# Kernel tuning notes

Hardware: AMD Instinct MI355X
Metric: run time of the kernel (lower is better)

## Reference

```python
import jax, jax.numpy as jnp
import numpy as np

KS = 3          # kernel_size
M = 6           # num_bases
TEM = 6         # tem_size = (KS//2)*num_bases
BN_EPS = 1e-3   # keras BatchNormalization default epsilon


def _conv(x, w):
    # x: NCHW, w: OIHW, stride 1, SAME padding (module uses padding='same')
    return jax.lax.conv_general_dilated(x, w, (1, 1), 'SAME',
                                        dimension_numbers=('NCHW', 'OIHW', 'NCHW'))


def _bn(x, gamma, beta, mean, var):
    # inference-mode batchnorm over channel dim (NCHW)
    s = gamma * jax.lax.rsqrt(var + BN_EPS)
    return x * s[None, :, None, None] + (beta - mean * s)[None, :, None, None]


def _unfold(x):
    # im2col: N,C,H,W -> N,C,KS*KS,H,W with SAME padding, stride 1
    N, C, H, W = x.shape
    xp = jnp.pad(x, ((0, 0), (0, 0), (1, 1), (1, 1)))
    taps = [xp[:, :, i:i + H, j:j + W] for i in range(KS) for j in range(KS)]
    return jnp.stack(taps, axis=2)


def setup_inputs() -> dict:
    key = jax.random.key(0)
    ks = jax.random.split(key, 16)
    N, C, O, H, W = 16, 128, 128, 64, 64
    inter, bsz = 64, M * TEM  # 64, 36
    x = jax.random.normal(ks[0], (N, C, H, W), jnp.float32)
    w1 = jax.random.normal(ks[1], (inter, C, 3, 3), jnp.float32) * (1.0 / np.sqrt(C * 9))
    gamma1 = jnp.ones((inter,), jnp.float32)
    beta1 = jnp.zeros((inter,), jnp.float32)
    mean1 = jax.random.normal(ks[2], (inter,), jnp.float32) * 0.1
    var1 = jax.random.uniform(ks[3], (inter,), jnp.float32, 0.5, 1.5)
    w2 = jax.random.normal(ks[4], (bsz, inter, 3, 3), jnp.float32) * (1.0 / np.sqrt(inter * 9))
    gamma2 = jnp.ones((bsz,), jnp.float32)
    beta2 = jnp.zeros((bsz,), jnp.float32)
    mean2 = jax.random.normal(ks[5], (bsz,), jnp.float32) * 0.1
    var2 = jax.random.uniform(ks[6], (bsz,), jnp.float32, 0.5, 1.5)
    # Fixed Fourier-Bessel-style basis [TEM, KS*KS], normalized as in calculate_FB_bases
    rng = np.random.RandomState(0)
    psi = rng.normal(size=(KS * KS, TEM)).astype(np.float32)
    c = np.sqrt((psi ** 2).sum(0).mean())
    fb_bases = jnp.asarray((psi / c).T)  # [TEM, 9]
    coef = jax.random.normal(ks[7], (O, C * M), jnp.float32) * np.sqrt(2.0 / (C * M))
    bias = jnp.zeros((O,), jnp.float32)
    return {'x': x, 'w1': w1, 'gamma1': gamma1, 'beta1': beta1, 'mean1': mean1,
            'var1': var1, 'w2': w2, 'gamma2': gamma2, 'beta2': beta2,
            'mean2': mean2, 'var2': var2, 'fb_bases': fb_bases, 'coef': coef,
            'bias': bias}


def reference(x, w1, gamma1, beta1, mean1, var1, w2, gamma2, beta2, mean2, var2,
              fb_bases, coef, bias):
    N, C, H, W = x.shape
    # bases_net: conv3x3 -> BN -> tanh -> conv3x3 -> BN -> tanh
    h = jnp.tanh(_bn(_conv(x, w1), gamma1, beta1, mean1, var1))
    b = jnp.tanh(_bn(_conv(h, w2), gamma2, beta2, mean2, var2))   # N,36,H,W
    bcoef = b.reshape(N, M, TEM, H, W)
    # combine predicted coefficients with fixed FB bases -> per-pixel filters
    bases = jnp.einsum('bmkhw,kl->bmlhw', bcoef, fb_bases)        # N,M,9,H,W
    xu = _unfold(x)                                               # N,C,9,H,W
    # per-pixel gather-multiply-reduce over the 9 taps
    bo = jnp.einsum('bmlhw,bclhw->bcmhw', bases, xu)              # N,C,M,H,W
    bo = bo.reshape(N, C * M, H, W)
    # 1x1 conv with coef + bias
    out = jnp.einsum('bkhw,ok->bohw', bo, coef) + bias[None, :, None, None]
    return out
```

## Files before the change

### kernel.cpp

```cpp
#include <hip/hip_runtime.h>
#include <hip/hip_bf16.h>

using bf16 = __hip_bfloat16;
typedef __attribute__((ext_vector_type(8))) short bf16x8;
typedef __attribute__((ext_vector_type(4))) float f32x4;
typedef __attribute__((ext_vector_type(2))) float f32x2;

#define BN_EPS 1e-3f

#define OFF_W1M   16u
#define OFF_B1F   36880u
#define OFF_W2M   36944u
#define OFF_B2F   50768u
#define OFF_FBF   50804u
#define OFF_CFM   50860u
#define OFF_BIASF 100012u
#define OFF_BB    100144u

__device__ __forceinline__ int dtype_flag(const void* g1) {
    return ((const unsigned*)g1)[0] != 0x3F800000u;
}

__device__ __forceinline__ float b2f(bf16 v) { return __bfloat162float(v); }
__device__ __forceinline__ unsigned short f2b(float f) {
    union { bf16 h; unsigned short u; } cv;
    cv.h = __float2bfloat16(f);
    return cv.u;
}
__device__ __forceinline__ unsigned packbf(float a, float b) {
    return (unsigned)f2b(a) | ((unsigned)f2b(b) << 16);
}
__device__ __forceinline__ float ldin(const void* p, long long i, int f) {
    return f ? b2f(((const bf16*)p)[i]) : ((const float*)p)[i];
}
__device__ __forceinline__ float lo_f(unsigned u) { return __uint_as_float(u << 16); }
__device__ __forceinline__ float hi_f(unsigned u) { return __uint_as_float(u & 0xFFFF0000u); }
__device__ __forceinline__ void ld8f(const void* p, long long i, int f, float* o) {
    if (f) {
        uint4 v = *(const uint4*)((const unsigned short*)p + i);
        o[0] = lo_f(v.x); o[1] = hi_f(v.x); o[2] = lo_f(v.y); o[3] = hi_f(v.y);
        o[4] = lo_f(v.z); o[5] = hi_f(v.z); o[6] = lo_f(v.w); o[7] = hi_f(v.w);
    } else {
        const float* q = (const float*)p + i;
        float4 a = *(const float4*)q, b = *(const float4*)(q + 4);
        o[0] = a.x; o[1] = a.y; o[2] = a.z; o[3] = a.w;
        o[4] = b.x; o[5] = b.y; o[6] = b.z; o[7] = b.w;
    }
}
__device__ __forceinline__ bf16x8 lds_frag(const unsigned short* p) {
    uint2 lo = *(const uint2*)p;
    uint2 hi = *(const uint2*)(p + 4);
    union { unsigned u[4]; bf16x8 v; } r;
    r.u[0] = lo.x; r.u[1] = lo.y; r.u[2] = hi.x; r.u[3] = hi.y;
    return r.v;
}

__global__ __launch_bounds__(256) void prep_kernel(
    const void* __restrict__ w1, const void* __restrict__ g1, const void* __restrict__ be1,
    const void* __restrict__ mu1, const void* __restrict__ va1,
    const void* __restrict__ w2, const void* __restrict__ g2, const void* __restrict__ be2,
    const void* __restrict__ mu2, const void* __restrict__ va2,
    const void* __restrict__ fb, const void* __restrict__ coef, const void* __restrict__ bias,
    float* __restrict__ ws)
{
    const int f = dtype_flag(g1);
    int j = blockIdx.x * 256 + threadIdx.x;
    if (j < 73728) {
        int tap = j >> 13, r = j & 8191;
        int ntile = r >> 11, r2 = r & 2047;
        int ks = r2 >> 9, r3 = r2 & 511;
        int lane = r3 >> 3, jj = r3 & 7;
        int oc = ntile * 16 + (lane & 15);
        int ic = ks * 32 + (lane >> 4) * 8 + jj;
        float s = ldin(g1, oc, f) * rsqrtf(ldin(va1, oc, f) + BN_EPS);
        ((unsigned short*)(ws + OFF_W1M))[j] = f2b(ldin(w1, (oc * 128 + ic) * 9 + tap, f) * s);
        return;
    }
    j -= 73728;
    if (j < 64) {
        float s = ldin(g1, j, f) * rsqrtf(ldin(va1, j, f) + BN_EPS);
        ws[OFF_B1F + j] = ldin(be1, j, f) - ldin(mu1, j, f) * s;
        return;
    }
    j -= 64;
    if (j < 27648) {
        int tap = j / 3072, r = j - tap * 3072;
        int ntile = r >> 10, r2 = r & 1023;
        int ks = r2 >> 9, r3 = r2 & 511;
        int lane = r3 >> 3, jj = r3 & 7;
        int oc = ntile * 16 + (lane & 15);
        int ic = ks * 32 + (lane >> 4) * 8 + jj;
        float v = 0.f;
        if (oc < 36) {
            float s = ldin(g2, oc, f) * rsqrtf(ldin(va2, oc, f) + BN_EPS);
            v = ldin(w2, (oc * 64 + ic) * 9 + tap, f) * s;
        }
        ((unsigned short*)(ws + OFF_W2M))[j] = f2b(v);
        return;
    }
    j -= 27648;
    if (j < 36) {
        float s = ldin(g2, j, f) * rsqrtf(ldin(va2, j, f) + BN_EPS);
        ws[OFF_B2F + j] = ldin(be2, j, f) - ldin(mu2, j, f) * s;
        return;
    }
    j -= 36;
    if (j < 54) { ws[OFF_FBF + j] = ldin(fb, j, f); return; }
    j -= 54;
    if (j < 98304) {
        int chunk = j / 12288, r = j - chunk * 12288;
        int ks = r >> 12, r2 = r & 4095;
        int ntile = r2 >> 9, r3 = r2 & 511;
        int lane = r3 >> 3, jj = r3 & 7;
        int o = ntile * 16 + (lane & 15);
        int k = chunk * 96 + ks * 32 + (lane >> 4) * 8 + jj;
        ((unsigned short*)(ws + OFF_CFM))[j] = f2b(ldin(coef, o * 768 + k, f));
        return;
    }
    j -= 98304;
    if (j < 128) { ws[OFF_BIASF + j] = ldin(bias, j, f); return; }
}

__global__ __launch_bounds__(512, 8) void conv1_mfma(
    const void* __restrict__ x, const void* __restrict__ g1, const float* __restrict__ ws,
    unsigned short* __restrict__ hbuf)
{
    __shared__ unsigned short sA[4][66][68];
    unsigned* sAu = (unsigned*)sA;
    const unsigned short* w1m = (const unsigned short*)(ws + OFF_W1M);
    const int f = dtype_flag(g1);
    const int t = threadIdx.x;
    const int n = blockIdx.x >> 5, h0 = (blockIdx.x & 31) * 2;

    for (int e = t; e < 272; e += 512) {
        int dy = e / 68, q = e - dy * 68;
        int wrow = (q >= 34) ? 65 : 0;
        int cu = (q >= 34) ? q - 34 : q;
        sAu[(dy * 66 + wrow) * 34 + cu] = 0u;
    }

    const int wv = t >> 6, lane = t & 63;
    const int fr = lane & 15, quad = lane >> 4;
    const int lr = wv >> 2;
    const int wcol = (wv & 3) * 16;

    f32x4 acc[4];
#pragma unroll
    for (int i = 0; i < 4; ++i) acc[i] = (f32x4){0.f, 0.f, 0.f, 0.f};

    const long long xb = (long long)n * 128 * 4096;
#pragma unroll
    for (int ph = 0; ph < 2; ++ph) {
        for (int u = t; u < 1024; u += 512) {
            int dy = u >> 8, rem = u & 255, icp = rem >> 3, w8 = rem & 7;
            int hh = h0 + dy - 1;
            float va[8], vb[8];
            if (hh >= 0 && hh < 64) {
                long long base = xb + (long long)(ph * 64 + icp * 2) * 4096 + hh * 64 + w8 * 8;
                ld8f(x, base, f, va);
                ld8f(x, base + 4096, f, vb);
            } else {
#pragma unroll
                for (int i = 0; i < 8; ++i) { va[i] = 0.f; vb[i] = 0.f; }
            }
            const int wb_ = w8 * 8 + 1;
#pragma unroll
            for (int i = 0; i < 8; ++i)
                sAu[(dy * 66 + wb_ + i) * 34 + icp] = packbf(va[i], vb[i]);
        }
        __syncthreads();
#pragma unroll
        for (int tap = 0; tap < 9; ++tap) {
            const int tdy = tap / 3, dx = tap - tdy * 3;
            const int dyr = lr + tdy;
#pragma unroll
            for (int ks = 0; ks < 2; ++ks) {
                const int kof = ks * 32 + quad * 8;
                const int kg = ph * 2 + ks;
                bf16x8 a = lds_frag(&sA[dyr][wcol + fr + dx][kof]);
#pragma unroll
                for (int nt = 0; nt < 4; ++nt) {
                    bf16x8 b = *(const bf16x8*)(w1m + (((tap * 4 + nt) * 4 + kg) * 64 + lane) * 8);
                    acc[nt] = __builtin_amdgcn_mfma_f32_16x16x32_bf16(a, b, acc[nt], 0, 0, 0);
                }
            }
        }
        if (ph == 0) __syncthreads();
    }

    const int w0 = wcol + quad * 4;
#pragma unroll
    for (int nt = 0; nt < 4; ++nt) {
        int oc = nt * 16 + fr;
        float bv = ws[OFF_B1F + oc];
        f32x4 v = acc[nt];
        union { unsigned short us[4]; uint2 u; } pk;
#pragma unroll
        for (int i = 0; i < 4; ++i) pk.us[i] = f2b(tanhf(v[i] + bv));
        *(uint2*)(hbuf + (size_t)(n * 64 + oc) * 4096 + (h0 + lr) * 64 + w0) = pk.u;
    }
}

__global__ __launch_bounds__(512, 8) void conv2_mfma(
    const float* __restrict__ ws, const unsigned short* __restrict__ hbuf,
    float* __restrict__ bbout)
{
    __shared__ unsigned short sA[4][66][68];
    unsigned* sAu = (unsigned*)sA;
    const unsigned short* w2m = (const unsigned short*)(ws + OFF_W2M);
    const int t = threadIdx.x;
    const int n = blockIdx.x >> 5, h0 = (blockIdx.x & 31) * 2;

    for (int e = t; e < 272; e += 512) {
        int dy = e / 68, q = e - dy * 68;
        int wrow = (q >= 34) ? 65 : 0;
        int cu = (q >= 34) ? q - 34 : q;
        sAu[(dy * 66 + wrow) * 34 + cu] = 0u;
    }
    {
        const unsigned short* hn = hbuf + (size_t)n * 64 * 4096;
        for (int u = t; u < 1024; u += 512) {
            int dy = u >> 8, rem = u & 255, icp = rem >> 3, w8 = rem & 7;
            int hh = h0 + dy - 1;
            uint4 a = make_uint4(0u, 0u, 0u, 0u), b = a;
            if (hh >= 0 && hh < 64) {
                const unsigned short* p = hn + (size_t)(icp * 2) * 4096 + hh * 64 + w8 * 8;
                a = *(const uint4*)p;
                b = *(const uint4*)(p + 4096);
            }
            const int wb_ = w8 * 8 + 1;
            unsigned au[4] = {a.x, a.y, a.z, a.w}, bu[4] = {b.x, b.y, b.z, b.w};
#pragma unroll
            for (int jj = 0; jj < 4; ++jj) {
                unsigned lo = (au[jj] & 0xFFFFu) | (bu[jj] << 16);
                unsigned hi = (au[jj] >> 16) | (bu[jj] & 0xFFFF0000u);
                sAu[(dy * 66 + wb_ + 2 * jj) * 34 + icp] = lo;
                sAu[(dy * 66 + wb_ + 2 * jj + 1) * 34 + icp] = hi;
            }
        }
    }
    __syncthreads();

    const int wv = t >> 6, lane = t & 63;
    const int fr = lane & 15, quad = lane >> 4;
    const int lr = wv >> 2;
    const int wcol = (wv & 3) * 16;

    f32x4 acc[3];
#pragma unroll
    for (int i = 0; i < 3; ++i) acc[i] = (f32x4){0.f, 0.f, 0.f, 0.f};

#pragma unroll
    for (int tap = 0; tap < 9; ++tap) {
        const int tdy = tap / 3, dx = tap - tdy * 3;
        const int dyr = lr + tdy;
#pragma unroll
        for (int ks = 0; ks < 2; ++ks) {
            const int kof = ks * 32 + quad * 8;
            bf16x8 a = lds_frag(&sA[dyr][wcol + fr + dx][kof]);
#pragma unroll
            for (int nt = 0; nt < 3; ++nt) {
                bf16x8 b = *(const bf16x8*)(w2m + (((tap * 3 + nt) * 2 + ks) * 64 + lane) * 8);
                acc[nt] = __builtin_amdgcn_mfma_f32_16x16x32_bf16(a, b, acc[nt], 0, 0, 0);
            }
        }
    }

    const int pbase = (n << 12) + (h0 + lr) * 64 + wcol + quad * 4;
#pragma unroll
    for (int nt = 0; nt < 2; ++nt) {
        int oc = nt * 16 + fr;
        float bv = ws[OFF_B2F + oc];
        f32x4 v = acc[nt];
#pragma unroll
        for (int reg = 0; reg < 4; ++reg)
            bbout[(size_t)(pbase + reg) * 36 + oc] = tanhf(v[reg] + bv);
    }
    if (fr < 4) {
        int oc = 32 + fr;
        float bv = ws[OFF_B2F + oc];
        f32x4 v = acc[2];
#pragma unroll
        for (int reg = 0; reg < 4; ++reg)
            bbout[(size_t)(pbase + reg) * 36 + oc] = tanhf(v[reg] + bv);
    }
}

__global__ __launch_bounds__(512, 8) void fuse_kernel(
    const void* __restrict__ x, const void* __restrict__ g1, const float* __restrict__ ws,
    void* __restrict__ outv)
{
    __shared__ float sbT[64][60];
    __shared__ __align__(16) unsigned short slbo[64][104];
    __shared__ __align__(16) unsigned short sX[3][66][22];
    unsigned* sXu = (unsigned*)sX;

    const float* bbp = ws + OFF_BB;
    const float* fbf = ws + OFF_FBF;
    const unsigned short* cfm = (const unsigned short*)(ws + OFF_CFM);
    const int f = dtype_flag(g1);

    const int t = threadIdx.x;
    const int p0 = blockIdx.x * 64;
    const int n = p0 >> 12;
    const int h = (p0 >> 6) & 63;

    const long long xbase = (long long)n * 128 * 4096;
    const int sw = t & 63, sg = t >> 6;

    float rv0[3], rv1[3];
#pragma unroll
    for (int dy = 0; dy < 3; ++dy) {
        int hh = h + dy - 1;
        float v0 = 0.f, v1 = 0.f;
        if (hh >= 0 && hh < 64) {
            long long base = xbase + (long long)(sg * 2) * 4096 + hh * 64 + sw;
            v0 = ldin(x, base, f);
            v1 = ldin(x, base + 4096, f);
        }
        rv0[dy] = v0; rv1[dy] = v1;
    }

    for (int task = t; task < 64 * 54; task += 512) {
        int p = task & 63, j = task >> 6;
        int m = j / 9, l = j - m * 9;
        const float* br = bbp + (size_t)(p0 + p) * 36 + m * 6;
        float s = 0.f;
#pragma unroll
        for (int k = 0; k < 6; ++k) s += br[k] * fbf[k * 9 + l];
        sbT[p][l * 6 + m] = s;
    }
    if (t < 66) {
        int dy = t / 22, q = t - dy * 22;
        int wrow = (q >= 11) ? 65 : 0;
        int cu = (q >= 11) ? q - 11 : q;
        sXu[(dy * 66 + wrow) * 11 + cu] = 0u;
    }

    const int pp = t >> 3, cl = t & 7;
    const int wv = t >> 6, lane = t & 63;
    const int fr = lane & 15, quad = lane >> 4;
    const int m0w = (wv & 3) * 16;
    const int nh = (wv >> 2) * 64;
    const int ntb = nh >> 4;

    f32x4 acc[4];
#pragma unroll
    for (int nt = 0; nt < 4; ++nt) acc[nt] = (f32x4){0.f, 0.f, 0.f, 0.f};

    __syncthreads();

#pragma unroll
    for (int chunk = 0; chunk < 8; ++chunk) {
#pragma unroll
        for (int dy = 0; dy < 3; ++dy)
            sXu[(dy * 66 + sw + 1) * 11 + sg] = packbf(rv0[dy], rv1[dy]);
        __syncthreads();
        if (chunk < 7) {
            const int c0n = (chunk + 1) * 16;
#pragma unroll
            for (int dy = 0; dy < 3; ++dy) {
                int hh = h + dy - 1;
                float v0 = 0.f, v1 = 0.f;
                if (hh >= 0 && hh < 64) {
                    long long base = xbase + (long long)(c0n + sg * 2) * 4096 + hh * 64 + sw;
                    v0 = ldin(x, base, f);
                    v1 = ldin(x, base + 4096, f);
                }
                rv0[dy] = v0; rv1[dy] = v1;
            }
        }
        {
            f32x2 xv[9];
#pragma unroll
            for (int dy = 0; dy < 3; ++dy)
#pragma unroll
                for (int dx = 0; dx < 3; ++dx) {
                    unsigned d = sXu[(dy * 66 + pp + dx) * 11 + cl];
                    xv[dy * 3 + dx] = (f32x2){lo_f(d), hi_f(d)};
                }
            f32x2 sm2[6];
#pragma unroll
            for (int m = 0; m < 6; ++m) sm2[m] = (f32x2){0.f, 0.f};
            const float* sp = &sbT[pp][0];
#pragma unroll
            for (int jv = 0; jv < 13; ++jv) {
                f32x4 s4 = *(const f32x4*)(sp + jv * 4);
#pragma unroll
                for (int e = 0; e < 4; ++e) {
                    const int j = jv * 4 + e;
                    const int l = j / 6, m = j - l * 6;
                    sm2[m] += xv[l] * s4[e];
                }
            }
            {
                f32x2 s2 = *(const f32x2*)(sp + 52);
                sm2[4] += xv[8] * s2[0];
                sm2[5] += xv[8] * s2[1];
            }
            unsigned* du = (unsigned*)slbo + pp * 52 + cl * 6;
            uint2 w0 = make_uint2(packbf(sm2[0][0], sm2[1][0]), packbf(sm2[2][0], sm2[3][0]));
            uint2 w1 = make_uint2(packbf(sm2[4][0], sm2[5][0]), packbf(sm2[0][1], sm2[1][1]));
            uint2 w2 = make_uint2(packbf(sm2[2][1], sm2[3][1]), packbf(sm2[4][1], sm2[5][1]));
            *(uint2*)&du[0] = w0;
            *(uint2*)&du[2] = w1;
            *(uint2*)&du[4] = w2;
        }
        __syncthreads();
#pragma unroll
        for (int ks = 0; ks < 3; ++ks) {
            const int kof = ks * 32 + quad * 8;
            bf16x8 a = *(const bf16x8*)&slbo[m0w + fr][kof];
            const unsigned short* cb = cfm + ((chunk * 3 + ks) * 8 + ntb) * 512 + lane * 8;
            bf16x8 b0 = *(const bf16x8*)(cb);
            bf16x8 b1 = *(const bf16x8*)(cb + 512);
            bf16x8 b2 = *(const bf16x8*)(cb + 1024);
            bf16x8 b3 = *(const bf16x8*)(cb + 1536);
            acc[0] = __builtin_amdgcn_mfma_f32_16x16x32_bf16(a, b0, acc[0], 0, 0, 0);
            acc[1] = __builtin_amdgcn_mfma_f32_16x16x32_bf16(a, b1, acc[1], 0, 0, 0);
            acc[2] = __builtin_amdgcn_mfma_f32_16x16x32_bf16(a, b2, acc[2], 0, 0, 0);
            acc[3] = __builtin_amdgcn_mfma_f32_16x16x32_bf16(a, b3, acc[3], 0, 0, 0);
        }
    }

    const int mrow = m0w + quad * 4;
#pragma unroll
    for (int nt = 0; nt < 4; ++nt) {
        int o = nh + nt * 16 + fr;
        float bv = ws[OFF_BIASF + o];
        f32x4 v = acc[nt];
        size_t ofs = (size_t)(n * 128 + o) * 4096 + h * 64 + mrow;
        if (f) {
            union { unsigned short us[4]; uint2 u; } pk;
#pragma unroll
            for (int i = 0; i < 4; ++i) pk.us[i] = f2b(v[i] + bv);
            *(uint2*)((unsigned short*)outv + ofs) = pk.u;
        } else {
            float4 w4 = make_float4(v[0] + bv, v[1] + bv, v[2] + bv, v[3] + bv);
            *(float4*)((float*)outv + ofs) = w4;
        }
    }
}

extern "C" void kernel_launch(void* const* d_in, const int* in_sizes, int n_in,
                              void* d_out, int out_size, void* d_ws, size_t ws_size,
                              hipStream_t stream)
{
    float* ws = (float*)d_ws;
    unsigned short* hbuf = (unsigned short*)d_out;

    hipLaunchKernelGGL(prep_kernel, dim3(782), dim3(256), 0, stream,
                       d_in[1], d_in[2], d_in[3], d_in[4], d_in[5],
                       d_in[6], d_in[7], d_in[8], d_in[9], d_in[10],
                       d_in[11], d_in[12], d_in[13], ws);
    hipLaunchKernelGGL(conv1_mfma, dim3(512), dim3(512), 0, stream, d_in[0], d_in[2], ws, hbuf);
    hipLaunchKernelGGL(conv2_mfma, dim3(512), dim3(512), 0, stream, ws, hbuf, ws + OFF_BB);
    hipLaunchKernelGGL(fuse_kernel, dim3(1024), dim3(512), 0, stream, d_in[0], d_in[2], ws, d_out);
}
```

Before: 199.4 us.

## Store intermediate activations channel-last and swap MFMA operands for vectorized stores

```diff
diff --git a/kernel.cpp b/kernel.cpp
--- a/kernel.cpp
+++ b/kernel.cpp
@@ -177,27 +177,28 @@
             for (int ks = 0; ks < 2; ++ks) {
                 const int kof = ks * 32 + quad * 8;
                 const int kg = ph * 2 + ks;
-                bf16x8 a = lds_frag(&sA[dyr][wcol + fr + dx][kof]);
+                bf16x8 px = lds_frag(&sA[dyr][wcol + fr + dx][kof]);
 #pragma unroll
                 for (int nt = 0; nt < 4; ++nt) {
-                    bf16x8 b = *(const bf16x8*)(w1m + (((tap * 4 + nt) * 4 + kg) * 64 + lane) * 8);
-                    acc[nt] = __builtin_amdgcn_mfma_f32_16x16x32_bf16(a, b, acc[nt], 0, 0, 0);
+                    bf16x8 wt = *(const bf16x8*)(w1m + (((tap * 4 + nt) * 4 + kg) * 64 + lane) * 8);
+                    acc[nt] = __builtin_amdgcn_mfma_f32_16x16x32_bf16(wt, px, acc[nt], 0, 0, 0);
                 }
             }
         }
         if (ph == 0) __syncthreads();
     }
 
-    const int w0 = wcol + quad * 4;
+    const size_t pixbase = (((size_t)n * 64 + h0 + lr) * 64 + wcol + fr) * 64;
+    const int ocb = quad * 4;
 #pragma unroll
     for (int nt = 0; nt < 4; ++nt) {
-        int oc = nt * 16 + fr;
-        float bv = ws[OFF_B1F + oc];
+        int oc0 = nt * 16 + ocb;
+        f32x4 bv = *(const f32x4*)(ws + OFF_B1F + oc0);
         f32x4 v = acc[nt];
         union { unsigned short us[4]; uint2 u; } pk;
 #pragma unroll
-        for (int i = 0; i < 4; ++i) pk.us[i] = f2b(tanhf(v[i] + bv));
-        *(uint2*)(hbuf + (size_t)(n * 64 + oc) * 4096 + (h0 + lr) * 64 + w0) = pk.u;
+        for (int i = 0; i < 4; ++i) pk.us[i] = f2b(tanhf(v[i] + bv[i]));
+        *(uint2*)(hbuf + pixbase + oc0) = pk.u;
     }
 }
 
@@ -205,38 +206,24 @@
     const float* __restrict__ ws, const unsigned short* __restrict__ hbuf,
     float* __restrict__ bbout)
 {
-    __shared__ unsigned short sA[4][66][68];
-    unsigned* sAu = (unsigned*)sA;
+    __shared__ __align__(16) unsigned short sA[4][66][72];
     const unsigned short* w2m = (const unsigned short*)(ws + OFF_W2M);
     const int t = threadIdx.x;
     const int n = blockIdx.x >> 5, h0 = (blockIdx.x & 31) * 2;
 
-    for (int e = t; e < 272; e += 512) {
-        int dy = e / 68, q = e - dy * 68;
-        int wrow = (q >= 34) ? 65 : 0;
-        int cu = (q >= 34) ? q - 34 : q;
-        sAu[(dy * 66 + wrow) * 34 + cu] = 0u;
+    if (t < 64) {
+        int dy = t >> 4, side = (t >> 3) & 1, c = t & 7;
+        *(uint4*)&sA[dy][side ? 65 : 0][c * 8] = make_uint4(0u, 0u, 0u, 0u);
     }
     {
-        const unsigned short* hn = hbuf + (size_t)n * 64 * 4096;
-        for (int u = t; u < 1024; u += 512) {
-            int dy = u >> 8, rem = u & 255, icp = rem >> 3, w8 = rem & 7;
+        const unsigned short* hn = hbuf + (size_t)n * 64 * 64 * 64;
+        for (int u = t; u < 2048; u += 512) {
+            int dy = u >> 9, rem = u & 511, w = rem >> 3, c8 = rem & 7;
             int hh = h0 + dy - 1;
-            uint4 a = make_uint4(0u, 0u, 0u, 0u), b = a;
-            if (hh >= 0 && hh < 64) {
-                const unsigned short* p = hn + (size_t)(icp * 2) * 4096 + hh * 64 + w8 * 8;
-                a = *(const uint4*)p;
-                b = *(const uint4*)(p + 4096);
-            }
-            const int wb_ = w8 * 8 + 1;
-            unsigned au[4] = {a.x, a.y, a.z, a.w}, bu[4] = {b.x, b.y, b.z, b.w};
-#pragma unroll
-            for (int jj = 0; jj < 4; ++jj) {
-                unsigned lo = (au[jj] & 0xFFFFu) | (bu[jj] << 16);
-                unsigned hi = (au[jj] >> 16) | (bu[jj] & 0xFFFF0000u);
-                sAu[(dy * 66 + wb_ + 2 * jj) * 34 + icp] = lo;
-                sAu[(dy * 66 + wb_ + 2 * jj + 1) * 34 + icp] = hi;
-            }
+            uint4 a = make_uint4(0u, 0u, 0u, 0u);
+            if (hh >= 0 && hh < 64)
+                a = *(const uint4*)(hn + (((size_t)hh * 64) + w) * 64 + c8 * 8);
+            *(uint4*)&sA[dy][w + 1][c8 * 8] = a;
         }
     }
     __syncthreads();
@@ -257,32 +244,27 @@
 #pragma unroll
         for (int ks = 0; ks < 2; ++ks) {
             const int kof = ks * 32 + quad * 8;
-            bf16x8 a = lds_frag(&sA[dyr][wcol + fr + dx][kof]);
+            bf16x8 px = lds_frag(&sA[dyr][wcol + fr + dx][kof]);
 #pragma unroll
             for (int nt = 0; nt < 3; ++nt) {
-                bf16x8 b = *(const bf16x8*)(w2m + (((tap * 3 + nt) * 2 + ks) * 64 + lane) * 8);
-                acc[nt] = __builtin_amdgcn_mfma_f32_16x16x32_bf16(a, b, acc[nt], 0, 0, 0);
-            }
-        }
-    }
-
-    const int pbase = (n << 12) + (h0 + lr) * 64 + wcol + quad * 4;
-#pragma unroll
-    for (int nt = 0; nt < 2; ++nt) {
-        int oc = nt * 16 + fr;
-        float bv = ws[OFF_B2F + oc];
-        f32x4 v = acc[nt];
-#pragma unroll
-        for (int reg = 0; reg < 4; ++reg)
-            bbout[(size_t)(pbase + reg) * 36 + oc] = tanhf(v[reg] + bv);
-    }
-    if (fr < 4) {
-        int oc = 32 + fr;
-        float bv = ws[OFF_B2F + oc];
-        f32x4 v = acc[2];
-#pragma unroll
-        for (int reg = 0; reg < 4; ++reg)
-            bbout[(size_t)(pbase + reg) * 36 + oc] = tanhf(v[reg] + bv);
+                bf16x8 wt = *(const bf16x8*)(w2m + (((tap * 3 + nt) * 2 + ks) * 64 + lane) * 8);
+                acc[nt] = __builtin_amdgcn_mfma_f32_16x16x32_bf16(wt, px, acc[nt], 0, 0, 0);
+            }
+        }
+    }
+
+    const size_t pix = (size_t)(n << 12) + (h0 + lr) * 64 + wcol + fr;
+    const int ocb = quad * 4;
+#pragma unroll
+    for (int nt = 0; nt < 3; ++nt) {
+        int oc0 = nt * 16 + ocb;
+        if (oc0 < 36) {
+            f32x4 bv = *(const f32x4*)(ws + OFF_B2F + oc0);
+            f32x4 v = acc[nt];
+            float4 st = make_float4(tanhf(v[0] + bv[0]), tanhf(v[1] + bv[1]),
+                                    tanhf(v[2] + bv[2]), tanhf(v[3] + bv[3]));
+            *(float4*)(bbout + pix * 36 + oc0) = st;
+        }
     }
 }
 
```

After: 205.9 us. 1.03x slower.
